# Performance work log

Hardware: AMD Instinct MI355X
Metric: run time of the kernel (lower is better)

Reference implementation:

```python
import jax, jax.numpy as jnp
import numpy as np

N_NODES = 100000
N_EDGES = 1600000
D_FEAT = 256
HID = 128
DEG_DIM = 128  # data.degree_exist_matrix.shape[1]


def setup_inputs() -> dict:
    key = jax.random.key(0)
    ks = jax.random.split(key, 12)
    s = lambda fan_in: 1.0 / np.sqrt(fan_in)
    x = jax.random.normal(ks[0], (N_NODES, D_FEAT), dtype=jnp.float32)
    edge_index = jax.random.randint(ks[1], (2, N_EDGES), 0, N_NODES, dtype=jnp.int32)
    return {
        "x": x,
        "edge_index": edge_index,
        # GCNConv 1 / 2 (PyG stores weight [in,out], bias [out])
        "W1": jax.random.uniform(ks[2], (D_FEAT, HID), jnp.float32, -s(D_FEAT), s(D_FEAT)),
        "b1": jnp.zeros((HID,), jnp.float32),
        "W2": jax.random.uniform(ks[3], (HID, HID), jnp.float32, -s(HID), s(HID)),
        "b2": jnp.zeros((HID,), jnp.float32),
        # down_sample Linear(D_FEAT, HID)
        "Wd": jax.random.uniform(ks[4], (D_FEAT, HID), jnp.float32, -s(D_FEAT), s(D_FEAT)),
        "bd": jax.random.uniform(ks[5], (HID,), jnp.float32, -s(D_FEAT), s(D_FEAT)),
        # linear2: Degree_layer(HID, 1) ~ Linear(HID, 1)
        "Wdeg": jax.random.uniform(ks[6], (HID, 1), jnp.float32, -s(HID), s(HID)),
        "bdeg": jax.random.uniform(ks[7], (1,), jnp.float32, -s(HID), s(HID)),
        # linear3: Linear(HID, DEG_DIM)
        "W3": jax.random.uniform(ks[8], (HID, DEG_DIM), jnp.float32, -s(HID), s(HID)),
        "b3": jax.random.uniform(ks[9], (DEG_DIM,), jnp.float32, -s(HID), s(HID)),
    }


def gcn_conv(x, W, b, src, dst, n):
    """PyG GCNConv: D^-1/2 (A+I) D^-1/2 X W + b (symmetric norm, self-loops)."""
    h = x @ W  # [N, out]
    deg = jax.ops.segment_sum(jnp.ones_like(dst, dtype=h.dtype), dst, num_segments=n) + 1.0
    dinv = jax.lax.rsqrt(deg)  # deg >= 1 from self loop
    coef = dinv[src] * dinv[dst]  # [E]
    msgs = h[src] * coef[:, None]  # [E, out] -- dominant gather
    agg = jax.ops.segment_sum(msgs, dst, num_segments=n)
    agg = agg + h * (dinv * dinv)[:, None]  # self-loop contribution
    return agg + b


def reference(x, edge_index, W1, b1, W2, b2, Wd, bd, Wdeg, bdeg, W3, b3):
    n = x.shape[0]
    src, dst = edge_index[0], edge_index[1]
    original_x = x @ Wd + bd
    h = gcn_conv(x, W1, b1, src, dst, n)
    h = jax.nn.relu(h)  # dropout is identity in eval mode
    h = gcn_conv(h, W2, b2, src, dst, n)
    h = h + original_x  # residual
    result1 = jax.nn.log_softmax(h, axis=-1)        # [N, HID]
    result2 = (h @ Wdeg + bdeg).squeeze(-1)          # [N]
    result3 = h @ W3 + b3                            # [N, DEG_DIM]
    return (result1, result2, result3)
```

## Files before the change

kernel.cpp:

```cpp
#include <hip/hip_runtime.h>


typedef __attribute__((ext_vector_type(8))) short bf16x8;
typedef __attribute__((ext_vector_type(4))) float f32x4;

#define CDIV(a, b) (((a) + (b) - 1) / (b))

#define GLOBAL_AS __attribute__((address_space(1)))
#define LDS_AS __attribute__((address_space(3)))

__device__ __forceinline__ void gload16(const void* g, void* l) {
  __builtin_amdgcn_global_load_lds((const GLOBAL_AS unsigned int*)g,
                                   (LDS_AS unsigned int*)l, 16, 0, 0);
}

__device__ __forceinline__ float b2f(unsigned short u) {
  union { unsigned int i; float f; } x; x.i = ((unsigned int)u) << 16; return x.f;
}
__device__ __forceinline__ unsigned short f2b(float f) {
  union { float f; unsigned int i; } x; x.f = f;
  unsigned int r = x.i + 0x7fffu + ((x.i >> 16) & 1u);
  return (unsigned short)(r >> 16);
}
__device__ __forceinline__ void add2(float& a0, float& a1, unsigned int u) {
  union { unsigned int i; float f; } lo, hi;
  lo.i = u << 16; hi.i = u & 0xffff0000u;
  a0 += lo.f; a1 += hi.f;
}
__device__ __forceinline__ unsigned int pack2(float lo, float hi) {
  return __builtin_amdgcn_perm(__float_as_uint(hi) + 0x8000u,
                               __float_as_uint(lo) + 0x8000u, 0x07060302u);
}


__global__ void k_wtrans4(const float* __restrict__ W1, const float* __restrict__ Wd,
                          const float* __restrict__ W2, const float* __restrict__ W3,
                          unsigned short* __restrict__ W1t, unsigned short* __restrict__ Wdt,
                          unsigned short* __restrict__ W2t, unsigned short* __restrict__ W3t) {
  int idx = blockIdx.x * blockDim.x + threadIdx.x;
  const float* in; unsigned short* out; int K, N;
  if (idx < 32768)       { in = W1; out = W1t; K = 256; N = 128; }
  else if (idx < 65536)  { in = Wd; out = Wdt; K = 256; N = 128; idx -= 32768; }
  else if (idx < 81920)  { in = W2; out = W2t; K = 128; N = 128; idx -= 65536; }
  else if (idx < 98304)  { in = W3; out = W3t; K = 128; N = 128; idx -= 81920; }
  else return;
  int k = idx / N, n = idx - k * N;
  out[n * K + k] = f2b(in[idx]);
}

__global__ void k_scan1(const int* __restrict__ deg, int* __restrict__ lscan,
                        int* __restrict__ partials, float* __restrict__ dinv, int n) {
  __shared__ int sd[256];
  int tid = threadIdx.x;
  int base = blockIdx.x * 2048 + tid * 8;
  int v[8]; int tsum = 0;
#pragma unroll
  for (int i = 0; i < 8; ++i) {
    int idx = base + i;
    int xv = (idx < n) ? deg[idx] : 0;
    v[i] = xv; tsum += xv;
    if (idx < n) dinv[idx] = 1.0f / sqrtf((float)xv + 1.0f);
  }
  sd[tid] = tsum;
  __syncthreads();
  for (int off = 1; off < 256; off <<= 1) {
    int t = (tid >= off) ? sd[tid - off] : 0;
    __syncthreads();
    sd[tid] += t;
    __syncthreads();
  }
  int run = sd[tid] - tsum;
#pragma unroll
  for (int i = 0; i < 8; ++i) {
    int idx = base + i;
    if (idx < n) lscan[idx] = run;
    run += v[i];
  }
  if (tid == 255) partials[blockIdx.x] = sd[255];
}

__global__ void k_scan2(const int* __restrict__ partials, int* __restrict__ pprefix, int nb) {
  if (threadIdx.x == 0 && blockIdx.x == 0) {
    int run = 0;
    for (int i = 0; i < nb; ++i) { pprefix[i] = run; run += partials[i]; }
    pprefix[nb] = run;
  }
}

__global__ void k_scan3(const int* __restrict__ pprefix, int* row_start,
                        int* __restrict__ cursor, int n, int E) {
  int idx = blockIdx.x * blockDim.x + threadIdx.x;
  if (idx >= n) return;
  int v = row_start[idx] + pprefix[idx >> 11];
  row_start[idx] = v;
  cursor[idx] = v;
  if (idx == 0) row_start[n] = E;
}


#define BIN_CHUNK 4096
#define OVF_CAP 65536

__global__ __launch_bounds__(256) void k_binA(
    const int* __restrict__ ei, int E, int nbuck, int cap,
    int* __restrict__ deg, int2* __restrict__ pairs, int* __restrict__ bcnt,
    int2* __restrict__ ovf, int* __restrict__ ovf_cnt) {
  __shared__ int lcnt[256];
  __shared__ int lbase[256];
  int tid = threadIdx.x;
  for (int i = tid; i < nbuck; i += 256) lcnt[i] = 0;
  __syncthreads();
  int base_e = blockIdx.x * BIN_CHUNK;
  int src[16], dst[16], lofs[16];
#pragma unroll
  for (int i = 0; i < 16; ++i) {
    int e = base_e + i * 256 + tid;
    if (e < E) {
      int s = ei[e], d = ei[E + e];
      src[i] = s; dst[i] = d;
      atomicAdd(&deg[d], 1);
      lofs[i] = atomicAdd(&lcnt[d >> 9], 1);
    } else {
      dst[i] = -1;
    }
  }
  __syncthreads();
  for (int b = tid; b < nbuck; b += 256)
    lbase[b] = atomicAdd(&bcnt[b], lcnt[b]);
  __syncthreads();
#pragma unroll
  for (int i = 0; i < 16; ++i) {
    if (dst[i] < 0) continue;
    int b = dst[i] >> 9;
    int gpos = lbase[b] + lofs[i];
    if (gpos < cap) {
      pairs[(size_t)b * cap + gpos] = make_int2(src[i], dst[i]);
    } else {
      int op = atomicAdd(ovf_cnt, 1);
      if (op < OVF_CAP) ovf[op] = make_int2(src[i], dst[i]);
    }
  }
}

__global__ __launch_bounds__(256) void k_binB(
    const int2* __restrict__ pairs, const int* __restrict__ bcnt,
    int nbuck, int cap,
    const int2* __restrict__ ovf, const int* __restrict__ ovf_cnt,
    int* __restrict__ cursor, int* __restrict__ csr_src) {
  if ((int)blockIdx.x < nbuck) {
    int b = blockIdx.x;
    int cnt = bcnt[b]; if (cnt > cap) cnt = cap;
    const int2* p = pairs + (size_t)b * cap;
    for (int i = threadIdx.x; i < cnt; i += 256) {
      int2 e = p[i];
      int pos = atomicAdd(&cursor[e.y], 1);
      csr_src[pos] = e.x;
    }
  } else {
    int total = *ovf_cnt; if (total > OVF_CAP) total = OVF_CAP;
    int start = (blockIdx.x - nbuck) * 256 + threadIdx.x;
    for (int i = start; i < total; i += 8 * 256) {
      int2 e = ovf[i];
      int pos = atomicAdd(&cursor[e.y], 1);
      csr_src[pos] = e.x;
    }
  }
}


__global__ __launch_bounds__(512) void k_gemm_x2(
    const float* __restrict__ X,
    const unsigned short* __restrict__ B1t,
    const unsigned short* __restrict__ B2t,
    const float* __restrict__ bias2,
    const float* __restrict__ dinvp,
    unsigned short* __restrict__ O1, float* __restrict__ O2, int n) {
  __shared__ char lds[65536];
  const int flat = threadIdx.x;
  const int wave = flat >> 6, lane = flat & 63;
  const int l15 = lane & 15, q = lane >> 4;
  const int wM = wave >> 1, wN = wave & 1;
  const int rowBase = blockIdx.x * 128;
  const int colBase = wN * 64;

  auto stage = [&](int kb, int buf) {
    char* ldsA = lds + buf * 32768;
    char* ldsB = ldsA + 16384;
    const char* Xb = (const char*)X;
#pragma unroll
    for (int j = 0; j < 2; ++j) {
      int i = j * 512 + flat;
      int row = i >> 3, pslot = i & 7;
      int lslot = pslot ^ (row & 7);
      int rowc = rowBase + row; if (rowc >= n) rowc = n - 1;
      gload16(Xb + (size_t)rowc * 1024 + (size_t)(kb * 128 + lslot * 16),
              ldsA + (j * 512 + wave * 64) * 16);
    }
#pragma unroll
    for (int j = 0; j < 2; ++j) {
      int i = j * 512 + flat;
      int col = i >> 3, pslot = i & 7;
      int lslot = pslot ^ (col & 7);
      const char* src = (lslot >= 4) ? (const char*)B2t : (const char*)B1t;
      gload16(src + (size_t)col * 512 + kb * 64 + (lslot & 3) * 16,
              ldsB + (j * 512 + wave * 64) * 16);
    }
  };

  f32x4 acc1[2][4], acc2[2][4];
#pragma unroll
  for (int i = 0; i < 2; ++i)
#pragma unroll
    for (int j = 0; j < 4; ++j) {
      acc1[i][j] = (f32x4){0.f, 0.f, 0.f, 0.f};
      acc2[i][j] = (f32x4){0.f, 0.f, 0.f, 0.f};
    }

  stage(0, 0);
  stage(1, 1);

#pragma unroll
  for (int kb = 0; kb < 8; ++kb) {
    int cur = kb & 1;
    if (kb < 7) asm volatile("s_waitcnt vmcnt(4)" ::: "memory");
    else        asm volatile("s_waitcnt vmcnt(0)" ::: "memory");
    __builtin_amdgcn_s_barrier();
    char* ldsA = lds + cur * 32768;
    char* ldsB = ldsA + 16384;
    bf16x8 a[2], b1v[4], b2v[4];
#pragma unroll
    for (int mt = 0; mt < 2; ++mt) {
      int row = wM * 32 + mt * 16 + l15;
      uint4 lo = *(const uint4*)(ldsA + row * 128 + (((2 * q) ^ (row & 7)) * 16));
      uint4 hi = *(const uint4*)(ldsA + row * 128 + (((2 * q + 1) ^ (row & 7)) * 16));
      union { bf16x8 v; unsigned int u[4]; } r;
      r.u[0] = __builtin_amdgcn_perm(lo.y + 0x8000u, lo.x + 0x8000u, 0x07060302u);
      r.u[1] = __builtin_amdgcn_perm(lo.w + 0x8000u, lo.z + 0x8000u, 0x07060302u);
      r.u[2] = __builtin_amdgcn_perm(hi.y + 0x8000u, hi.x + 0x8000u, 0x07060302u);
      r.u[3] = __builtin_amdgcn_perm(hi.w + 0x8000u, hi.z + 0x8000u, 0x07060302u);
      a[mt] = r.v;
    }
#pragma unroll
    for (int nt = 0; nt < 4; ++nt) {
      int col = colBase + nt * 16 + l15;
      b1v[nt] = *(const bf16x8*)(ldsB + col * 128 + ((q ^ (col & 7)) * 16));
      b2v[nt] = *(const bf16x8*)(ldsB + col * 128 + (((4 + q) ^ (col & 7)) * 16));
    }
#pragma unroll
    for (int mt = 0; mt < 2; ++mt)
#pragma unroll
      for (int nt = 0; nt < 4; ++nt) {
        acc1[mt][nt] = __builtin_amdgcn_mfma_f32_16x16x32_bf16(a[mt], b1v[nt], acc1[mt][nt], 0, 0, 0);
        acc2[mt][nt] = __builtin_amdgcn_mfma_f32_16x16x32_bf16(a[mt], b2v[nt], acc2[mt][nt], 0, 0, 0);
      }
    asm volatile("s_waitcnt lgkmcnt(0)" ::: "memory");
    __builtin_amdgcn_s_barrier();
    if (kb < 6) stage(kb + 2, cur);
  }

#pragma unroll
  for (int mt = 0; mt < 2; ++mt) {
    float4 dv = *(const float4*)(dinvp + rowBase + wM * 32 + mt * 16 + q * 4);
#pragma unroll
    for (int nt = 0; nt < 4; ++nt) {
      int col = colBase + nt * 16 + l15;
      float bb = bias2[col];
#pragma unroll
      for (int r = 0; r < 4; ++r) {
        int row = rowBase + wM * 32 + mt * 16 + q * 4 + r;
        if (row < n) {
          float dvr = (r == 0) ? dv.x : (r == 1) ? dv.y : (r == 2) ? dv.z : dv.w;
          O1[(size_t)row * 128 + col] = f2b(acc1[mt][nt][r] * dvr);
          O2[(size_t)row * 128 + col] = acc2[mt][nt][r] + bb;
        }
      }
    }
  }
}

template <int OUT_F32>
__global__ __launch_bounds__(512) void k_gemm_h(
    const unsigned short* __restrict__ X, const unsigned short* __restrict__ Bt,
    const float* __restrict__ bias, const float* __restrict__ dinvp,
    unsigned short* __restrict__ Ob, float* __restrict__ Of, int n) {
  __shared__ char lds[65536];
  const int flat = threadIdx.x;
  const int wave = flat >> 6, lane = flat & 63;
  const int l15 = lane & 15, q = lane >> 4;
  const int wM = wave >> 1, wN = wave & 1;
  const int rowBase = blockIdx.x * 128;
  const int colBase = wN * 64;

  auto stage = [&](int ks, int buf) {
    char* ldsA = lds + buf * 32768;
    char* ldsB = ldsA + 16384;
#pragma unroll
    for (int j = 0; j < 2; ++j) {
      int i = j * 512 + flat;
      int row = i >> 3, pslot = i & 7;
      int lslot = pslot ^ (row & 7);
      int rowc = rowBase + row; if (rowc >= n) rowc = n - 1;
      gload16((const char*)X + (size_t)rowc * 256 + ks * 128 + lslot * 16,
              ldsA + (j * 512 + wave * 64) * 16);
    }
#pragma unroll
    for (int j = 0; j < 2; ++j) {
      int i = j * 512 + flat;
      int col = i >> 3, pslot = i & 7;
      int lslot = pslot ^ (col & 7);
      gload16((const char*)Bt + (size_t)col * 256 + ks * 128 + lslot * 16,
              ldsB + (j * 512 + wave * 64) * 16);
    }
  };

  f32x4 acc[2][4];
#pragma unroll
  for (int i = 0; i < 2; ++i)
#pragma unroll
    for (int j = 0; j < 4; ++j) acc[i][j] = (f32x4){0.f, 0.f, 0.f, 0.f};

  stage(0, 0);
  stage(1, 1);

#pragma unroll
  for (int ks = 0; ks < 2; ++ks) {
    if (ks == 0) asm volatile("s_waitcnt vmcnt(4)" ::: "memory");
    else         asm volatile("s_waitcnt vmcnt(0)" ::: "memory");
    __builtin_amdgcn_s_barrier();
    char* ldsA = lds + ks * 32768;
    char* ldsB = ldsA + 16384;
#pragma unroll
    for (int k2 = 0; k2 < 2; ++k2) {
      bf16x8 a[2], b[4];
#pragma unroll
      for (int mt = 0; mt < 2; ++mt) {
        int row = wM * 32 + mt * 16 + l15;
        a[mt] = *(const bf16x8*)(ldsA + row * 128 + (((k2 * 4 + q) ^ (row & 7)) * 16));
      }
#pragma unroll
      for (int nt = 0; nt < 4; ++nt) {
        int col = colBase + nt * 16 + l15;
        b[nt] = *(const bf16x8*)(ldsB + col * 128 + (((k2 * 4 + q) ^ (col & 7)) * 16));
      }
#pragma unroll
      for (int mt = 0; mt < 2; ++mt)
#pragma unroll
        for (int nt = 0; nt < 4; ++nt)
          acc[mt][nt] = __builtin_amdgcn_mfma_f32_16x16x32_bf16(a[mt], b[nt], acc[mt][nt], 0, 0, 0);
    }
  }

#pragma unroll
  for (int mt = 0; mt < 2; ++mt) {
    float4 dv;
    if (!OUT_F32) dv = *(const float4*)(dinvp + rowBase + wM * 32 + mt * 16 + q * 4);
#pragma unroll
    for (int nt = 0; nt < 4; ++nt) {
      int col = colBase + nt * 16 + l15;
      float bb = OUT_F32 ? bias[col] : 0.f;
#pragma unroll
      for (int r = 0; r < 4; ++r) {
        int row = rowBase + wM * 32 + mt * 16 + q * 4 + r;
        if (row < n) {
          if (OUT_F32) {
            __builtin_nontemporal_store(acc[mt][nt][r] + bb, &Of[(size_t)row * 128 + col]);
          } else {
            float dvr = (r == 0) ? dv.x : (r == 1) ? dv.y : (r == 2) ? dv.z : dv.w;
            Ob[(size_t)row * 128 + col] = f2b(acc[mt][nt][r] * dvr);
          }
        }
      }
    }
  }
}


__device__ __forceinline__ void agg_edges4(
    const unsigned short* __restrict__ h, const int* __restrict__ csr_src,
    int beg, int end, int lane, int grp, int sub, float* acc) {
  for (int base = beg; base < end; base += 64) {
    int m = end - base; if (m > 64) m = 64;
    int idx_l = (base + lane < end) ? csr_src[base + lane] : 0;
    for (int j = 0; j < m; j += 16) {
      int s0 = __builtin_amdgcn_ds_bpermute((j + grp) << 2, idx_l);
      int s1 = __builtin_amdgcn_ds_bpermute((j + 4 + grp) << 2, idx_l);
      int s2 = __builtin_amdgcn_ds_bpermute((j + 8 + grp) << 2, idx_l);
      int s3 = __builtin_amdgcn_ds_bpermute((j + 12 + grp) << 2, idx_l);
      uint4 v0 = *(const uint4*)(h + (size_t)s0 * 128 + sub * 8);
      uint4 v1 = *(const uint4*)(h + (size_t)s1 * 128 + sub * 8);
      uint4 v2 = *(const uint4*)(h + (size_t)s2 * 128 + sub * 8);
      uint4 v3 = *(const uint4*)(h + (size_t)s3 * 128 + sub * 8);
      if (j + grp < m) {
        add2(acc[0], acc[1], v0.x); add2(acc[2], acc[3], v0.y);
        add2(acc[4], acc[5], v0.z); add2(acc[6], acc[7], v0.w);
      }
      if (j + 4 + grp < m) {
        add2(acc[0], acc[1], v1.x); add2(acc[2], acc[3], v1.y);
        add2(acc[4], acc[5], v1.z); add2(acc[6], acc[7], v1.w);
      }
      if (j + 8 + grp < m) {
        add2(acc[0], acc[1], v2.x); add2(acc[2], acc[3], v2.y);
        add2(acc[4], acc[5], v2.z); add2(acc[6], acc[7], v2.w);
      }
      if (j + 12 + grp < m) {
        add2(acc[0], acc[1], v3.x); add2(acc[2], acc[3], v3.y);
        add2(acc[4], acc[5], v3.z); add2(acc[6], acc[7], v3.w);
      }
    }
  }
}

__device__ __forceinline__ void grp_reduce(float* acc) {
#pragma unroll
  for (int i = 0; i < 8; ++i) {
    acc[i] += __shfl_xor(acc[i], 16);
    acc[i] += __shfl_xor(acc[i], 32);
  }
}

__global__ __launch_bounds__(256) void k_agg1(
    const unsigned short* __restrict__ h,
    const int* __restrict__ row_start, const int* __restrict__ csr_src,
    const float* __restrict__ dinv,
    const float* __restrict__ bias,
    unsigned short* __restrict__ hout, int n) {
  int gw = blockIdx.x * 4 + (threadIdx.x >> 6);
  int lane = threadIdx.x & 63;
  int grp = lane >> 4, sub = lane & 15;
  if (gw >= n) return;
  int beg = row_start[gw], end = row_start[gw + 1];
  float acc[8] = {0.f, 0.f, 0.f, 0.f, 0.f, 0.f, 0.f, 0.f};
  agg_edges4(h, csr_src, beg, end, lane, grp, sub, acc);
  grp_reduce(acc);
  if (grp == 0) {
    float dg = dinv[gw];
    uint4 sv = *(const uint4*)(h + (size_t)gw * 128 + sub * 8);
    add2(acc[0], acc[1], sv.x); add2(acc[2], acc[3], sv.y);
    add2(acc[4], acc[5], sv.z); add2(acc[6], acc[7], sv.w);
    float4 b0 = *(const float4*)(bias + sub * 8);
    float4 b1v = *(const float4*)(bias + sub * 8 + 4);
    float a[8];
    a[0] = fmaxf(acc[0] * dg + b0.x, 0.f); a[1] = fmaxf(acc[1] * dg + b0.y, 0.f);
    a[2] = fmaxf(acc[2] * dg + b0.z, 0.f); a[3] = fmaxf(acc[3] * dg + b0.w, 0.f);
    a[4] = fmaxf(acc[4] * dg + b1v.x, 0.f); a[5] = fmaxf(acc[5] * dg + b1v.y, 0.f);
    a[6] = fmaxf(acc[6] * dg + b1v.z, 0.f); a[7] = fmaxf(acc[7] * dg + b1v.w, 0.f);
    uint4 o;
    o.x = pack2(a[0], a[1]); o.y = pack2(a[2], a[3]);
    o.z = pack2(a[4], a[5]); o.w = pack2(a[6], a[7]);
    *(uint4*)(hout + (size_t)gw * 128 + sub * 8) = o;
  }
}

__global__ __launch_bounds__(256) void k_agg2_epi(
    const unsigned short* __restrict__ h,
    const int* __restrict__ row_start, const int* __restrict__ csr_src,
    const float* __restrict__ dinv,
    const float* __restrict__ bias,
    float* res_out1,
    const float* __restrict__ wdeg, const float* __restrict__ bdeg,
    float* __restrict__ out2,
    unsigned short* __restrict__ hf,
    int n) {
  int gw = blockIdx.x * 4 + (threadIdx.x >> 6);
  int lane = threadIdx.x & 63;
  int grp = lane >> 4, sub = lane & 15;
  if (gw >= n) return;
  int beg = row_start[gw], end = row_start[gw + 1];
  float acc[8] = {0.f, 0.f, 0.f, 0.f, 0.f, 0.f, 0.f, 0.f};
  agg_edges4(h, csr_src, beg, end, lane, grp, sub, acc);
  grp_reduce(acc);
  if (grp == 0) {
    float dg = dinv[gw];
    uint4 sv = *(const uint4*)(h + (size_t)gw * 128 + sub * 8);
    add2(acc[0], acc[1], sv.x); add2(acc[2], acc[3], sv.y);
    add2(acc[4], acc[5], sv.z); add2(acc[6], acc[7], sv.w);
    float4 b0 = *(const float4*)(bias + sub * 8);
    float4 b1v = *(const float4*)(bias + sub * 8 + 4);
    float4 r0 = *(const float4*)(res_out1 + (size_t)gw * 128 + sub * 8);
    float4 r1 = *(const float4*)(res_out1 + (size_t)gw * 128 + sub * 8 + 4);
    float a[8];
    a[0] = acc[0] * dg + b0.x + r0.x; a[1] = acc[1] * dg + b0.y + r0.y;
    a[2] = acc[2] * dg + b0.z + r0.z; a[3] = acc[3] * dg + b0.w + r0.w;
    a[4] = acc[4] * dg + b1v.x + r1.x; a[5] = acc[5] * dg + b1v.y + r1.y;
    a[6] = acc[6] * dg + b1v.z + r1.z; a[7] = acc[7] * dg + b1v.w + r1.w;
    uint4 o;
    o.x = pack2(a[0], a[1]); o.y = pack2(a[2], a[3]);
    o.z = pack2(a[4], a[5]); o.w = pack2(a[6], a[7]);
    *(uint4*)(hf + (size_t)gw * 128 + sub * 8) = o;
    float4 w0 = *(const float4*)(wdeg + sub * 8);
    float4 w1 = *(const float4*)(wdeg + sub * 8 + 4);
    float t = a[0] * w0.x + a[1] * w0.y + a[2] * w0.z + a[3] * w0.w +
              a[4] * w1.x + a[5] * w1.y + a[6] * w1.z + a[7] * w1.w;
#pragma unroll
    for (int mk = 8; mk >= 1; mk >>= 1) t += __shfl_xor(t, mk);
    if (sub == 0) __builtin_nontemporal_store(t + bdeg[0], out2 + gw);
    float mx = a[0];
#pragma unroll
    for (int i = 1; i < 8; ++i) mx = fmaxf(mx, a[i]);
#pragma unroll
    for (int mk = 8; mk >= 1; mk >>= 1) mx = fmaxf(mx, __shfl_xor(mx, mk));
    float l = 0.f;
#pragma unroll
    for (int i = 0; i < 8; ++i) l += __expf(a[i] - mx);
#pragma unroll
    for (int mk = 8; mk >= 1; mk >>= 1) l += __shfl_xor(l, mk);
    float ls = mx + __logf(l);
    f32x4 o0 = {a[0] - ls, a[1] - ls, a[2] - ls, a[3] - ls};
    f32x4 o1 = {a[4] - ls, a[5] - ls, a[6] - ls, a[7] - ls};
    __builtin_nontemporal_store(o0, (f32x4*)(res_out1 + (size_t)gw * 128 + sub * 8));
    __builtin_nontemporal_store(o1, (f32x4*)(res_out1 + (size_t)gw * 128 + sub * 8 + 4));
  }
}


extern "C" void kernel_launch(void* const* d_in, const int* in_sizes, int n_in,
                              void* d_out, int out_size, void* d_ws, size_t ws_size,
                              hipStream_t stream) {
  const float* x   = (const float*)d_in[0];
  const int*   ei  = (const int*)d_in[1];
  const float* W1  = (const float*)d_in[2];
  const float* b1  = (const float*)d_in[3];
  const float* W2  = (const float*)d_in[4];
  const float* b2  = (const float*)d_in[5];
  const float* Wd  = (const float*)d_in[6];
  const float* bd  = (const float*)d_in[7];
  const float* Wdg = (const float*)d_in[8];
  const float* bdg = (const float*)d_in[9];
  const float* W3  = (const float*)d_in[10];
  const float* b3  = (const float*)d_in[11];

  const int N = in_sizes[0] / 256;
  const int E = in_sizes[1] / 2;

  char* w = (char*)d_ws;
  auto alloc = [&](size_t bytes) {
    char* p = w;
    w += (bytes + 255) & ~(size_t)255;
    return p;
  };
  unsigned short* W1t  = (unsigned short*)alloc((size_t)256 * 128 * 2);
  unsigned short* Wdt  = (unsigned short*)alloc((size_t)256 * 128 * 2);
  unsigned short* W2t  = (unsigned short*)alloc((size_t)128 * 128 * 2);
  unsigned short* W3t  = (unsigned short*)alloc((size_t)128 * 128 * 2);
  unsigned short* bufC = (unsigned short*)alloc((size_t)N * 128 * 2);
  int*   deg      = (int*)alloc((size_t)N * 4);
  float* dinv     = (float*)alloc((size_t)(N + 128) * 4);
  int*   row_start= (int*)alloc((size_t)(N + 1) * 4);
  int*   cursor   = (int*)alloc((size_t)N * 4);
  int*   partials = (int*)alloc(4096);
  int*   pprefix  = (int*)alloc(4096);
  int*   csr_src  = (int*)alloc((size_t)E * 4);
  int*   bcnt     = (int*)alloc(2048);
  int*   ovf_cnt  = bcnt + 256;
  int2*  ovf      = (int2*)alloc((size_t)OVF_CAP * 8);

  float* out1 = (float*)d_out;
  float* out2 = out1 + (size_t)N * 128;
  float* out3 = out2 + (size_t)N;
  unsigned short* bufA = (unsigned short*)out3;

  const int nbuck = CDIV(N, 512);
  int cap = (E / nbuck) + (E / nbuck) / 2;
  cap = (cap + 255) & ~255;
  size_t bufC_bytes = (size_t)N * 128 * 2;
  if ((size_t)nbuck * cap * 8 > bufC_bytes)
    cap = (int)(bufC_bytes / ((size_t)nbuck * 8));
  int2* pairs = (int2*)bufC;

  hipMemsetAsync(deg, 0, (size_t)N * 4, stream);
  hipMemsetAsync(bcnt, 0, 2048, stream);

  k_wtrans4<<<CDIV(98304, 256), 256, 0, stream>>>(W1, Wd, W2, W3, W1t, Wdt, W2t, W3t);

  k_binA<<<CDIV(E, BIN_CHUNK), 256, 0, stream>>>(ei, E, nbuck, cap, deg, pairs,
                                                 bcnt, ovf, ovf_cnt);

  const int nb = CDIV(N, 2048);
  k_scan1<<<nb, 256, 0, stream>>>(deg, row_start, partials, dinv, N);
  k_scan2<<<1, 64, 0, stream>>>(partials, pprefix, nb);
  k_scan3<<<CDIV(N, 256), 256, 0, stream>>>(pprefix, row_start, cursor, N, E);

  k_gemm_x2<<<CDIV(N, 128), 512, 0, stream>>>(x, W1t, Wdt, bd, dinv, bufA, out1, N);

  k_binB<<<nbuck + 8, 256, 0, stream>>>(pairs, bcnt, nbuck, cap, ovf, ovf_cnt,
                                        cursor, csr_src);

  k_agg1<<<CDIV(N, 4), 256, 0, stream>>>(bufA, row_start, csr_src, dinv, b1, bufC, N);

  k_gemm_h<0><<<CDIV(N, 128), 512, 0, stream>>>(bufC, W2t, nullptr, dinv, bufA, nullptr, N);

  k_agg2_epi<<<CDIV(N, 4), 256, 0, stream>>>(bufA, row_start, csr_src, dinv,
                                             b2, out1, Wdg, bdg, out2, bufC, N);

  k_gemm_h<1><<<CDIV(N, 128), 512, 0, stream>>>(bufC, W3t, b3, nullptr, nullptr, out3, N);
}
```

Baseline: 529.6 us.

## Slice layer-1 features into 16-column planes for cache-local aggregation

The first GEMM now writes its bf16 output as eight column-slice planes of 16 features each, stored slice-major. The first aggregation launches one block group per slice, so each pass gathers from a 3.2 MB plane that can stay cache-resident instead of the full 25.6 MB feature matrix. The second GEMM is rewritten to read this sliced layout directly into registers, with only the weights staged in LDS. In exchange, edge indices and CSR offsets are re-read eight times and the launch is eight times larger, with 32-byte gathers per edge.

```diff
diff --git a/kernel.cpp b/kernel.cpp
--- a/kernel.cpp
+++ b/kernel.cpp
@@ -174,7 +174,8 @@
     const unsigned short* __restrict__ B2t,
     const float* __restrict__ bias2,
     const float* __restrict__ dinvp,
-    unsigned short* __restrict__ O1, float* __restrict__ O2, int n) {
+    unsigned short* __restrict__ O1,
+    float* __restrict__ O2, int n) {
   __shared__ char lds[65536];
   const int flat = threadIdx.x;
   const int wave = flat >> 6, lane = flat & 63;
@@ -264,13 +265,14 @@
 #pragma unroll
     for (int nt = 0; nt < 4; ++nt) {
       int col = colBase + nt * 16 + l15;
+      int slice = wN * 4 + nt;
       float bb = bias2[col];
 #pragma unroll
       for (int r = 0; r < 4; ++r) {
         int row = rowBase + wM * 32 + mt * 16 + q * 4 + r;
         if (row < n) {
           float dvr = (r == 0) ? dv.x : (r == 1) ? dv.y : (r == 2) ? dv.z : dv.w;
-          O1[(size_t)row * 128 + col] = f2b(acc1[mt][nt][r] * dvr);
+          O1[((size_t)slice * n + row) * 16 + l15] = f2b(acc1[mt][nt][r] * dvr);
           O2[(size_t)row * 128 + col] = acc2[mt][nt][r] + bb;
         }
       }
@@ -278,11 +280,90 @@
   }
 }
 
-template <int OUT_F32>
-__global__ __launch_bounds__(512) void k_gemm_h(
+__global__ __launch_bounds__(512) void k_gemm_h_sl(
+    const unsigned short* __restrict__ X,
+    const unsigned short* __restrict__ Bt,
+    const float* __restrict__ dinvp,
+    unsigned short* __restrict__ Ob, int n) {
+  __shared__ char lds[32768];
+  const int flat = threadIdx.x;
+  const int wave = flat >> 6, lane = flat & 63;
+  const int l15 = lane & 15, q = lane >> 4;
+  const int wM = wave >> 1, wN = wave & 1;
+  const int rowBase = blockIdx.x * 128 + wM * 32;
+  const int colBase = wN * 64;
+
+  int rowIdx[2];
+#pragma unroll
+  for (int mt = 0; mt < 2; ++mt) {
+    int r = rowBase + mt * 16 + l15;
+    rowIdx[mt] = (r < n) ? r : (n - 1);
+  }
+
+  uint4 a4[2][4];
+#pragma unroll
+  for (int mt = 0; mt < 2; ++mt)
+#pragma unroll
+    for (int kb = 0; kb < 4; ++kb) {
+      size_t off = ((size_t)(kb * 2 + (q >> 1)) * n + rowIdx[mt]) * 16 + (q & 1) * 8;
+      a4[mt][kb] = *(const uint4*)(X + off);
+    }
+
+#pragma unroll
+  for (int j = 0; j < 4; ++j) {
+    int i = j * 512 + flat;
+    int col = i >> 4, slot = i & 15;
+    int lslot = slot ^ (col & 7);
+    gload16((const char*)Bt + (size_t)col * 256 + lslot * 16,
+            lds + ((size_t)j * 512 + wave * 64) * 16);
+  }
+  __syncthreads();
+
+  f32x4 acc[2][4];
+#pragma unroll
+  for (int i = 0; i < 2; ++i)
+#pragma unroll
+    for (int j = 0; j < 4; ++j) acc[i][j] = (f32x4){0.f, 0.f, 0.f, 0.f};
+
+#pragma unroll
+  for (int kb = 0; kb < 4; ++kb) {
+    bf16x8 b[4];
+#pragma unroll
+    for (int nt = 0; nt < 4; ++nt) {
+      int col = colBase + nt * 16 + l15;
+      int s = (kb * 4 + q) ^ (col & 7);
+      b[nt] = *(const bf16x8*)(lds + (size_t)col * 256 + s * 16);
+    }
+#pragma unroll
+    for (int mt = 0; mt < 2; ++mt) {
+      bf16x8 a = *(const bf16x8*)&a4[mt][kb];
+#pragma unroll
+      for (int nt = 0; nt < 4; ++nt)
+        acc[mt][nt] = __builtin_amdgcn_mfma_f32_16x16x32_bf16(a, b[nt], acc[mt][nt], 0, 0, 0);
+    }
+  }
+
+#pragma unroll
+  for (int mt = 0; mt < 2; ++mt) {
+    float4 dv = *(const float4*)(dinvp + rowBase + mt * 16 + q * 4);
+#pragma unroll
+    for (int nt = 0; nt < 4; ++nt) {
+      int col = colBase + nt * 16 + l15;
+#pragma unroll
+      for (int r = 0; r < 4; ++r) {
+        int row = rowBase + mt * 16 + q * 4 + r;
+        if (row < n) {
+          float dvr = (r == 0) ? dv.x : (r == 1) ? dv.y : (r == 2) ? dv.z : dv.w;
+          Ob[(size_t)row * 128 + col] = f2b(acc[mt][nt][r] * dvr);
+        }
+      }
+    }
+  }
+}
+
+__global__ __launch_bounds__(512) void k_gemm_h_f32(
     const unsigned short* __restrict__ X, const unsigned short* __restrict__ Bt,
-    const float* __restrict__ bias, const float* __restrict__ dinvp,
-    unsigned short* __restrict__ Ob, float* __restrict__ Of, int n) {
+    const float* __restrict__ bias, float* __restrict__ Of, int n) {
   __shared__ char lds[65536];
   const int flat = threadIdx.x;
   const int wave = flat >> 6, lane = flat & 63;
@@ -351,29 +432,77 @@
   }
 
 #pragma unroll
-  for (int mt = 0; mt < 2; ++mt) {
-    float4 dv;
-    if (!OUT_F32) dv = *(const float4*)(dinvp + rowBase + wM * 32 + mt * 16 + q * 4);
+  for (int mt = 0; mt < 2; ++mt)
 #pragma unroll
     for (int nt = 0; nt < 4; ++nt) {
       int col = colBase + nt * 16 + l15;
-      float bb = OUT_F32 ? bias[col] : 0.f;
+      float bb = bias[col];
 #pragma unroll
       for (int r = 0; r < 4; ++r) {
         int row = rowBase + wM * 32 + mt * 16 + q * 4 + r;
-        if (row < n) {
-          if (OUT_F32) {
-            __builtin_nontemporal_store(acc[mt][nt][r] + bb, &Of[(size_t)row * 128 + col]);
-          } else {
-            float dvr = (r == 0) ? dv.x : (r == 1) ? dv.y : (r == 2) ? dv.z : dv.w;
-            Ob[(size_t)row * 128 + col] = f2b(acc[mt][nt][r] * dvr);
-          }
-        }
-      }
-    }
-  }
-}
-
+        if (row < n)
+          __builtin_nontemporal_store(acc[mt][nt][r] + bb, &Of[(size_t)row * 128 + col]);
+      }
+    }
+}
+
+
+__global__ __launch_bounds__(256) void k_agg1_sl(
+    const unsigned short* __restrict__ hA,
+    const int* __restrict__ row_start, const int* __restrict__ csr_src,
+    const float* __restrict__ dinv,
+    const float* __restrict__ bias,
+    unsigned short* __restrict__ hout,
+    int n) {
+  int s = blockIdx.x & 7;
+  int gw = (blockIdx.x >> 3) * 4 + (threadIdx.x >> 6);
+  int lane = threadIdx.x & 63;
+  int sub2 = lane & 1;
+  if (gw >= n) return;
+  int beg = row_start[gw], end = row_start[gw + 1];
+  const unsigned short* hs = hA + (size_t)s * n * 16;
+  float acc[8] = {0.f, 0.f, 0.f, 0.f, 0.f, 0.f, 0.f, 0.f};
+  for (int base = beg; base < end; base += 64) {
+    int idx_l = (base + lane < end) ? csr_src[base + lane] : 0;
+#pragma unroll
+    for (int j = 0; j < 64; j += 32) {
+      if (base + j >= end) break;
+      int e = j + (lane >> 1);
+      int se = __builtin_amdgcn_ds_bpermute(e << 2, idx_l);
+      uint4 v = *(const uint4*)(hs + (size_t)se * 16 + sub2 * 8);
+      if (base + e < end) {
+        add2(acc[0], acc[1], v.x); add2(acc[2], acc[3], v.y);
+        add2(acc[4], acc[5], v.z); add2(acc[6], acc[7], v.w);
+      }
+    }
+  }
+#pragma unroll
+  for (int i = 0; i < 8; ++i) {
+    acc[i] += __shfl_xor(acc[i], 2);
+    acc[i] += __shfl_xor(acc[i], 4);
+    acc[i] += __shfl_xor(acc[i], 8);
+    acc[i] += __shfl_xor(acc[i], 16);
+    acc[i] += __shfl_xor(acc[i], 32);
+  }
+  if (lane < 2) {
+    float dg = dinv[gw];
+    uint4 sv = *(const uint4*)(hs + (size_t)gw * 16 + sub2 * 8);
+    add2(acc[0], acc[1], sv.x); add2(acc[2], acc[3], sv.y);
+    add2(acc[4], acc[5], sv.z); add2(acc[6], acc[7], sv.w);
+    const float* bp = bias + s * 16 + sub2 * 8;
+    float4 b0 = *(const float4*)bp;
+    float4 b1v = *(const float4*)(bp + 4);
+    float a[8];
+    a[0] = fmaxf(acc[0] * dg + b0.x, 0.f); a[1] = fmaxf(acc[1] * dg + b0.y, 0.f);
+    a[2] = fmaxf(acc[2] * dg + b0.z, 0.f); a[3] = fmaxf(acc[3] * dg + b0.w, 0.f);
+    a[4] = fmaxf(acc[4] * dg + b1v.x, 0.f); a[5] = fmaxf(acc[5] * dg + b1v.y, 0.f);
+    a[6] = fmaxf(acc[6] * dg + b1v.z, 0.f); a[7] = fmaxf(acc[7] * dg + b1v.w, 0.f);
+    uint4 o;
+    o.x = pack2(a[0], a[1]); o.y = pack2(a[2], a[3]);
+    o.z = pack2(a[4], a[5]); o.w = pack2(a[6], a[7]);
+    *(uint4*)(hout + ((size_t)s * n + gw) * 16 + sub2 * 8) = o;
+  }
+}
 
 __device__ __forceinline__ void agg_edges4(
     const unsigned short* __restrict__ h, const int* __restrict__ csr_src,
@@ -410,47 +539,6 @@
   }
 }
 
-__device__ __forceinline__ void grp_reduce(float* acc) {
-#pragma unroll
-  for (int i = 0; i < 8; ++i) {
-    acc[i] += __shfl_xor(acc[i], 16);
-    acc[i] += __shfl_xor(acc[i], 32);
-  }
-}
-
-__global__ __launch_bounds__(256) void k_agg1(
-    const unsigned short* __restrict__ h,
-    const int* __restrict__ row_start, const int* __restrict__ csr_src,
-    const float* __restrict__ dinv,
-    const float* __restrict__ bias,
-    unsigned short* __restrict__ hout, int n) {
-  int gw = blockIdx.x * 4 + (threadIdx.x >> 6);
-  int lane = threadIdx.x & 63;
-  int grp = lane >> 4, sub = lane & 15;
-  if (gw >= n) return;
-  int beg = row_start[gw], end = row_start[gw + 1];
-  float acc[8] = {0.f, 0.f, 0.f, 0.f, 0.f, 0.f, 0.f, 0.f};
-  agg_edges4(h, csr_src, beg, end, lane, grp, sub, acc);
-  grp_reduce(acc);
-  if (grp == 0) {
-    float dg = dinv[gw];
-    uint4 sv = *(const uint4*)(h + (size_t)gw * 128 + sub * 8);
-    add2(acc[0], acc[1], sv.x); add2(acc[2], acc[3], sv.y);
-    add2(acc[4], acc[5], sv.z); add2(acc[6], acc[7], sv.w);
-    float4 b0 = *(const float4*)(bias + sub * 8);
-    float4 b1v = *(const float4*)(bias + sub * 8 + 4);
-    float a[8];
-    a[0] = fmaxf(acc[0] * dg + b0.x, 0.f); a[1] = fmaxf(acc[1] * dg + b0.y, 0.f);
-    a[2] = fmaxf(acc[2] * dg + b0.z, 0.f); a[3] = fmaxf(acc[3] * dg + b0.w, 0.f);
-    a[4] = fmaxf(acc[4] * dg + b1v.x, 0.f); a[5] = fmaxf(acc[5] * dg + b1v.y, 0.f);
-    a[6] = fmaxf(acc[6] * dg + b1v.z, 0.f); a[7] = fmaxf(acc[7] * dg + b1v.w, 0.f);
-    uint4 o;
-    o.x = pack2(a[0], a[1]); o.y = pack2(a[2], a[3]);
-    o.z = pack2(a[4], a[5]); o.w = pack2(a[6], a[7]);
-    *(uint4*)(hout + (size_t)gw * 128 + sub * 8) = o;
-  }
-}
-
 __global__ __launch_bounds__(256) void k_agg2_epi(
     const unsigned short* __restrict__ h,
     const int* __restrict__ row_start, const int* __restrict__ csr_src,
@@ -468,7 +556,11 @@
   int beg = row_start[gw], end = row_start[gw + 1];
   float acc[8] = {0.f, 0.f, 0.f, 0.f, 0.f, 0.f, 0.f, 0.f};
   agg_edges4(h, csr_src, beg, end, lane, grp, sub, acc);
-  grp_reduce(acc);
+#pragma unroll
+  for (int i = 0; i < 8; ++i) {
+    acc[i] += __shfl_xor(acc[i], 16);
+    acc[i] += __shfl_xor(acc[i], 32);
+  }
   if (grp == 0) {
     float dg = dinv[gw];
     uint4 sv = *(const uint4*)(h + (size_t)gw * 128 + sub * 8);
@@ -585,12 +677,13 @@
   k_binB<<<nbuck + 8, 256, 0, stream>>>(pairs, bcnt, nbuck, cap, ovf, ovf_cnt,
                                         cursor, csr_src);
 
-  k_agg1<<<CDIV(N, 4), 256, 0, stream>>>(bufA, row_start, csr_src, dinv, b1, bufC, N);
-
-  k_gemm_h<0><<<CDIV(N, 128), 512, 0, stream>>>(bufC, W2t, nullptr, dinv, bufA, nullptr, N);
+  k_agg1_sl<<<8 * CDIV(N, 4), 256, 0, stream>>>(bufA, row_start, csr_src, dinv,
+                                                b1, bufC, N);
+
+  k_gemm_h_sl<<<CDIV(N, 128), 512, 0, stream>>>(bufC, W2t, dinv, bufA, N);
 
   k_agg2_epi<<<CDIV(N, 4), 256, 0, stream>>>(bufA, row_start, csr_src, dinv,
                                              b2, out1, Wdg, bdg, out2, bufC, N);
 
-  k_gemm_h<1><<<CDIV(N, 128), 512, 0, stream>>>(bufC, W3t, b3, nullptr, nullptr, out3, N);
-}
+  k_gemm_h_f32<<<CDIV(N, 128), 512, 0, stream>>>(bufC, W3t, b3, out3, N);
+}
```

New measurement: 809.4 us. 52.8% more time.
